# Kernel optimization log

Measured on AMD Instinct MI355X. Metric: run time of the kernel, lower is better.

Reference implementation:

```python
import jax, jax.numpy as jnp
import numpy as np

NPOINT = 2048
K = 16
EPS = 1e-5


def farthest_point_sample(xyz, npoint):
    # xyz: (B, N, 3) -> (B, npoint) int32 indices. Deterministic start at index 0.
    B, N, _ = xyz.shape
    batch = jnp.arange(B)

    def step(carry, _):
        dists, far = carry                      # (B,N), (B,)
        centroid = xyz[batch, far]              # (B,3)
        d = jnp.sum((xyz - centroid[:, None, :]) ** 2, axis=-1)  # (B,N)
        dists = jnp.minimum(dists, d)
        nxt = jnp.argmax(dists, axis=-1).astype(jnp.int32)
        return (dists, nxt), far

    init = (jnp.full((B, N), 1e10, xyz.dtype), jnp.zeros((B,), jnp.int32))
    _, idx = jax.lax.scan(step, init, None, length=npoint)
    return jnp.transpose(idx)                   # (B, npoint)


def knn_query(k, xyz, query_xyz):
    # squared-distance KNN via matmul form (same ordering as torch.cdist+topk smallest)
    x2 = jnp.sum(xyz * xyz, axis=-1)            # (B,N)
    q2 = jnp.sum(query_xyz * query_xyz, axis=-1)  # (B,S)
    sqd = q2[:, :, None] + x2[:, None, :] - 2.0 * jnp.einsum('bsd,bnd->bsn', query_xyz, xyz)
    _, idx = jax.lax.top_k(-sqd, k)             # smallest k distances
    return idx                                  # (B,S,k)


def layer_norm(x, g, b):
    mu = jnp.mean(x, axis=-1, keepdims=True)
    var = jnp.mean((x - mu) ** 2, axis=-1, keepdims=True)
    return (x - mu) * jax.lax.rsqrt(var + EPS) * g + b


def setup_inputs() -> dict:
    key = jax.random.key(0)
    ks = jax.random.split(key, 6)
    B, N, IN_DIM, OUT_DIM = 4, 8192, 64, 128
    C_IN = 3 + IN_DIM
    s1 = 1.0 / np.sqrt(C_IN)
    s2 = 1.0 / np.sqrt(OUT_DIM)
    return {
        'xyz': jax.random.normal(ks[0], (B, N, 3), jnp.float32),
        'feat': jax.random.normal(ks[1], (B, N, IN_DIM), jnp.float32),
        'W1': jax.random.uniform(ks[2], (C_IN, OUT_DIM), jnp.float32, -s1, s1),
        'b1': jax.random.uniform(ks[3], (OUT_DIM,), jnp.float32, -s1, s1),
        'W2': jax.random.uniform(ks[4], (OUT_DIM, OUT_DIM), jnp.float32, -s2, s2),
        'b2': jax.random.uniform(ks[5], (OUT_DIM,), jnp.float32, -s2, s2),
        'ln_g': jnp.ones((OUT_DIM,), jnp.float32),
        'ln_b': jnp.zeros((OUT_DIM,), jnp.float32),
    }


def reference(xyz, feat, W1, b1, W2, b2, ln_g, ln_b):
    B = xyz.shape[0]
    bidx = jnp.arange(B)[:, None, None]

    fps_idx = farthest_point_sample(xyz, NPOINT)                 # (B,S)
    new_xyz = jnp.take_along_axis(xyz, fps_idx[:, :, None], axis=1)  # (B,S,3)
    knn_idx = knn_query(K, xyz, new_xyz)                         # (B,S,K)

    grp_xyz = xyz[bidx, knn_idx] - new_xyz[:, :, None, :]        # (B,S,K,3)
    grp_feat = feat[bidx, knn_idx]                               # (B,S,K,in_dim)
    grouped = jnp.concatenate([grp_xyz, grp_feat], axis=-1)      # (B,S,K,3+in_dim)

    h = jax.nn.relu(grouped @ W1 + b1)
    h = h @ W2 + b2                                              # (B,S,K,out_dim)
    new_feat = jnp.max(h, axis=2)                                # (B,S,out_dim)
    return new_xyz, layer_norm(new_feat, ln_g, ln_b)
```

## Files before the change

kernel.cpp:

```cpp
#include <hip/hip_runtime.h>
#include <stdint.h>

#define BB 4
#define NN 8192
#define SS 2048
#define KK 16
#define IND 64
#define CIN 67
#define OD 128

typedef unsigned int   u32;
typedef unsigned long long u64;
typedef float f2 __attribute__((ext_vector_type(2)));

__global__ __launch_bounds__(256) void k_prep(const float* __restrict__ xyz,
                                              float4* __restrict__ pts){
  int i = blockIdx.x * 256 + threadIdx.x;
  if (i >= BB*NN) return;
  float x = xyz[3*i+0];
  float y = xyz[3*i+1];
  float z = xyz[3*i+2];
  float x2 = __fadd_rn(__fadd_rn(__fmul_rn(x,x), __fmul_rn(y,y)), __fmul_rn(z,z));
  pts[i] = make_float4(x,y,z,x2);
}

template<int CTRL>
__device__ __forceinline__ float dpp_mv(float x){
  int xi = __builtin_bit_cast(int, x);
  int r  = __builtin_amdgcn_update_dpp(xi, xi, CTRL, 0xf, 0xf, false);
  return __builtin_bit_cast(float, r);
}

#define FPT 512
#define PPT (NN/FPT)
#define NW  (FPT/64)
#define FPS_LDS ((3*NN + 3*SS)*4)
__global__ __launch_bounds__(FPT, 2) void k_fps(const float4* __restrict__ pts,
                                                float* __restrict__ out_xyz){
  #pragma clang fp contract(off)
  extern __shared__ float smem[];
  float* sx = smem;
  float* sy = smem +   NN;
  float* sz = smem + 2*NN;
  float* rx = smem + 3*NN;
  float* ry = smem + 3*NN +   SS;
  float* rz = smem + 3*NN + 2*SS;
  __shared__ u64 pkey[2][NW];
  int b = blockIdx.x;
  int tid = threadIdx.x;
  int wid = tid >> 6, lane = tid & 63;
  const float4* P = pts + (size_t)b*NN;
  f2 X[PPT/2], Y[PPT/2], Z[PPT/2], D[PPT/2];
  #pragma unroll
  for (int jp=0;jp<PPT/2;jp++){
    int n0 = tid*PPT + 2*jp;
    float4 p0 = P[n0];
    float4 p1 = P[n0+1];
    X[jp] = (f2){p0.x, p1.x};
    Y[jp] = (f2){p0.y, p1.y};
    Z[jp] = (f2){p0.z, p1.z};
    D[jp] = (f2){1e10f, 1e10f};
    sx[n0]=p0.x; sx[n0+1]=p1.x;
    sy[n0]=p0.y; sy[n0+1]=p1.y;
    sz[n0]=p0.z; sz[n0+1]=p1.z;
  }
  float4 p0v = P[0];
  float cx=p0v.x, cy=p0v.y, cz=p0v.z;
  if (tid==0){ rx[0]=cx; ry[0]=cy; rz[0]=cz; }
  __syncthreads();

  for (int it=1; it<SS; ++it){
    f2 mm = (f2){-1.0f, -1.0f};
    #pragma unroll
    for (int jp=0;jp<PPT/2;jp++){
      f2 dx = X[jp] - cx;
      f2 dy = Y[jp] - cy;
      f2 dz = Z[jp] - cz;
      f2 d  = ((dx*dx) + (dy*dy)) + (dz*dz);
      f2 nd = __builtin_elementwise_min(D[jp], d);
      D[jp] = nd;
      mm = __builtin_elementwise_max(mm, nd);
    }
    float md = fmaxf(mm.x, mm.y);
    float m = md;
    m = fmaxf(m, dpp_mv<0x111>(m));
    m = fmaxf(m, dpp_mv<0x112>(m));
    m = fmaxf(m, dpp_mv<0x114>(m));
    m = fmaxf(m, dpp_mv<0x118>(m));
    m = fmaxf(m, dpp_mv<0x142>(m));
    m = fmaxf(m, dpp_mv<0x143>(m));
    float wmax = __builtin_bit_cast(float,
        __builtin_amdgcn_readlane(__builtin_bit_cast(int, m), 63));
    u64 ball = __ballot(md == wmax);
    int wl = __ffsll((unsigned long long)ball) - 1;
    int bj = 0;
    if (md == wmax){
      #pragma unroll
      for (int t=PPT-1;t>=0;--t){
        float v = (t&1)? D[t>>1].y : D[t>>1].x;
        if (v == wmax) bj = t;
      }
    }
    int widx = __shfl(tid*PPT + bj, wl, 64);
    if (lane==0){
      pkey[it&1][wid] = ((u64)__float_as_uint(wmax) << 32) | (u32)~(u32)widx;
    }
    __syncthreads();
    u64 bk = pkey[it&1][0];
    #pragma unroll
    for (int w=1;w<NW;w++){
      u64 k2 = pkey[it&1][w];
      if (k2 > bk) bk = k2;
    }
    int gw = (int)~(u32)bk;
    cx = sx[gw]; cy = sy[gw]; cz = sz[gw];
    if (tid==0){ rx[it]=cx; ry[it]=cy; rz[it]=cz; }
  }
  __syncthreads();
  for (int i=tid; i<SS; i+=FPT){
    size_t o = (size_t)b*SS*3 + (size_t)i*3;
    out_xyz[o]=rx[i]; out_xyz[o+1]=ry[i]; out_xyz[o+2]=rz[i];
  }
}

__global__ __launch_bounds__(256) void k_knn(const float4* __restrict__ pts,
                                             const float* __restrict__ ctr,
                                             int* __restrict__ knn_idx){
  int q = blockIdx.x*4 + (threadIdx.x>>6);
  int lane = threadIdx.x & 63;
  int b = q / SS;
  const float4* P = pts + (size_t)b*NN;
  float qx=ctr[3*q], qy=ctr[3*q+1], qz=ctr[3*q+2];
  float q2 = __fadd_rn(__fadd_rn(__fmul_rn(qx,qx),__fmul_rn(qy,qy)),__fmul_rn(qz,qz));
  u64 key[KK];
  #pragma unroll
  for (int t=0;t<KK;t++) key[t] = ~0ull;
  for (int i=0;i<NN/64;i++){
    int n = i*64 + lane;
    float4 p = P[n];
    float dot = __fadd_rn(__fadd_rn(__fmul_rn(qx,p.x),__fmul_rn(qy,p.y)),__fmul_rn(qz,p.z));
    float sd  = __fsub_rn(__fadd_rn(q2,p.w), __fmul_rn(2.0f,dot));
    u32 bu = __float_as_uint(sd);
    bu ^= (u32)((int)bu >> 31) | 0x80000000u;
    u64 kk = ((u64)bu<<32) | (u32)n;
    if (kk < key[KK-1]){
      key[KK-1] = kk;
      #pragma unroll
      for (int t=KK-1;t>0;--t){
        u64 a=key[t-1], c=key[t];
        bool sw = c < a;
        key[t-1] = sw? c : a;
        key[t]   = sw? a : c;
      }
    }
  }
  #pragma unroll 1
  for (int r=0;r<KK;r++){
    u64 m = key[0];
    #pragma unroll
    for (int mm=1;mm<64;mm<<=1){
      u64 om = __shfl_xor((unsigned long long)m, mm, 64);
      if (om < m) m = om;
    }
    if (lane==0) knn_idx[q*KK + r] = (int)(u32)m;
    if (key[0]==m){
      #pragma unroll
      for (int t=0;t<KK-1;t++) key[t]=key[t+1];
      key[KK-1]=~0ull;
    }
  }
}

__global__ __launch_bounds__(256) void k_mlp(const float* __restrict__ feat,
                                             const float4* __restrict__ pts,
                                             const float* __restrict__ ctr,
                                             const int* __restrict__ knn_idx,
                                             const float* __restrict__ W1, const float* __restrict__ b1,
                                             const float* __restrict__ W2, const float* __restrict__ b2,
                                             const float* __restrict__ g_ln, const float* __restrict__ b_ln,
                                             float* __restrict__ out_feat){
  __shared__ float gbuf[4][CIN][16];
  __shared__ float hbuf[4][OD][20];
  int wid = threadIdx.x>>6, lane = threadIdx.x&63;
  int q = blockIdx.x*4 + wid;
  int b = q / SS;
  float* gw = &gbuf[wid][0][0];
  float* hw = &hbuf[wid][0][0];
  int k = lane & 15, part = lane >> 4;
  int n = knn_idx[q*KK + k];
  {
    const float* fp = feat + ((size_t)b*NN + (size_t)n)*IND + part*16;
    float4 f0 = *(const float4*)(fp+0);
    float4 f1 = *(const float4*)(fp+4);
    float4 f2v = *(const float4*)(fp+8);
    float4 f3 = *(const float4*)(fp+12);
    float v[16] = {f0.x,f0.y,f0.z,f0.w, f1.x,f1.y,f1.z,f1.w,
                   f2v.x,f2v.y,f2v.z,f2v.w, f3.x,f3.y,f3.z,f3.w};
    #pragma unroll
    for (int c=0;c<16;c++) gw[(3+part*16+c)*16 + k] = v[c];
    if (part==0){
      float4 p = pts[(size_t)b*NN + n];
      gw[0*16+k] = __fsub_rn(p.x, ctr[3*q+0]);
      gw[1*16+k] = __fsub_rn(p.y, ctr[3*q+1]);
      gw[2*16+k] = __fsub_rn(p.z, ctr[3*q+2]);
    }
  }
  __syncthreads();
  int o = lane;
  float a0[16], a1[16];
  #pragma unroll
  for (int t=0;t<16;t++){ a0[t]=0.0f; a1[t]=0.0f; }
  #pragma unroll 4
  for (int j=0;j<CIN;j++){
    float w0 = W1[j*OD + o];
    float w1 = W1[j*OD + o + 64];
    #pragma unroll
    for (int t=0;t<16;t++){
      float gv = gw[j*16+t];
      a0[t]=fmaf(gv,w0,a0[t]); a1[t]=fmaf(gv,w1,a1[t]);
    }
  }
  float bb0 = b1[o], bb1 = b1[o+64];
  #pragma unroll
  for (int t=0;t<16;t++){
    hw[o*20+t]      = fmaxf(a0[t]+bb0, 0.0f);
    hw[(o+64)*20+t] = fmaxf(a1[t]+bb1, 0.0f);
  }
  __syncthreads();
  float c0[16], c1[16];
  #pragma unroll
  for (int t=0;t<16;t++){ c0[t]=0.0f; c1[t]=0.0f; }
  #pragma unroll 4
  for (int j=0;j<OD;j++){
    float w0 = W2[j*OD + o];
    float w1 = W2[j*OD + o + 64];
    #pragma unroll
    for (int t=0;t<16;t++){
      float hv = hw[j*20+t];
      c0[t]=fmaf(hv,w0,c0[t]); c1[t]=fmaf(hv,w1,c1[t]);
    }
  }
  float m0=c0[0], m1=c1[0];
  #pragma unroll
  for (int t=1;t<16;t++){ m0=fmaxf(m0,c0[t]); m1=fmaxf(m1,c1[t]); }
  m0 += b2[o]; m1 += b2[o+64];
  float ssum = m0+m1;
  #pragma unroll
  for (int mm=1;mm<64;mm<<=1) ssum += __shfl_xor(ssum,mm,64);
  float mean = ssum * (1.0f/128.0f);
  float d0=m0-mean, d1=m1-mean;
  float sq = d0*d0 + d1*d1;
  #pragma unroll
  for (int mm=1;mm<64;mm<<=1) sq += __shfl_xor(sq,mm,64);
  float var = sq * (1.0f/128.0f);
  float x = var + 1e-5f;
  float r = rsqrtf(x);
  r = r * (1.5f - 0.5f*x*r*r);
  size_t obf = (size_t)q*OD;
  out_feat[obf+o]    = fmaf(d0*r, g_ln[o],    b_ln[o]);
  out_feat[obf+o+64] = fmaf(d1*r, g_ln[o+64], b_ln[o+64]);
}

extern "C" void kernel_launch(void* const* d_in, const int* in_sizes, int n_in,
                              void* d_out, int out_size, void* d_ws, size_t ws_size,
                              hipStream_t stream){
  const float* xyz  = (const float*)d_in[0];
  const float* feat = (const float*)d_in[1];
  const float* W1   = (const float*)d_in[2];
  const float* b1   = (const float*)d_in[3];
  const float* W2   = (const float*)d_in[4];
  const float* b2   = (const float*)d_in[5];
  const float* lg   = (const float*)d_in[6];
  const float* lb   = (const float*)d_in[7];
  float* out = (float*)d_out;
  char* ws = (char*)d_ws;
  float4* pts = (float4*)ws;
  int*    kidx = (int*)(ws + 524288);
  float* out_xyz  = out;
  float* out_feat = out + (size_t)BB*SS*3;

  hipFuncSetAttribute((const void*)k_fps,
                      hipFuncAttributeMaxDynamicSharedMemorySize, FPS_LDS);

  hipLaunchKernelGGL(k_prep, dim3((BB*NN+255)/256), dim3(256), 0,       stream, xyz, pts);
  hipLaunchKernelGGL(k_fps,  dim3(BB),              dim3(FPT), FPS_LDS, stream, pts, out_xyz);
  hipLaunchKernelGGL(k_knn,  dim3(BB*SS/4),         dim3(256), 0,       stream, pts, out_xyz, kidx);
  hipLaunchKernelGGL(k_mlp,  dim3(BB*SS/4),         dim3(256), 0,       stream,
                     feat, pts, out_xyz, kidx, W1, b1, W2, b2, lg, lb, out_feat);
}
```

Before: 2.408 ms.

## Halve FPS block size, split max accumulators, and drop shuffle in argmax

The farthest-point-sampling kernel now runs with 256 threads per batch instead of 512, so each thread holds 32 points and there are 4 waves instead of 8. The per-iteration cross-wave reduction and barrier therefore involve fewer participants. The distance loop uses two independent max accumulators to shorten the dependency chain. The winning lane writes its key directly instead of going through a shuffle, and the 4-wave key reduction is written as a tree. In exchange, each thread does twice the per-iteration distance work and needs more registers, which could lengthen the serial critical path of the 2048-iteration loop.

```diff
diff --git a/kernel.cpp b/kernel.cpp
--- a/kernel.cpp
+++ b/kernel.cpp
@@ -31,11 +31,11 @@
   return __builtin_bit_cast(float, r);
 }
 
-#define FPT 512
+#define FPT 256
 #define PPT (NN/FPT)
 #define NW  (FPT/64)
 #define FPS_LDS ((3*NN + 3*SS)*4)
-__global__ __launch_bounds__(FPT, 2) void k_fps(const float4* __restrict__ pts,
+__global__ __launch_bounds__(FPT, 1) void k_fps(const float4* __restrict__ pts,
                                                 float* __restrict__ out_xyz){
   #pragma clang fp contract(off)
   extern __shared__ float smem[];
@@ -70,17 +70,21 @@
   __syncthreads();
 
   for (int it=1; it<SS; ++it){
-    f2 mm = (f2){-1.0f, -1.0f};
-    #pragma unroll
-    for (int jp=0;jp<PPT/2;jp++){
-      f2 dx = X[jp] - cx;
-      f2 dy = Y[jp] - cy;
-      f2 dz = Z[jp] - cz;
-      f2 d  = ((dx*dx) + (dy*dy)) + (dz*dz);
-      f2 nd = __builtin_elementwise_min(D[jp], d);
-      D[jp] = nd;
-      mm = __builtin_elementwise_max(mm, nd);
-    }
+    f2 mm0 = (f2){-1.0f, -1.0f}, mm1 = (f2){-1.0f, -1.0f};
+    #pragma unroll
+    for (int jp=0;jp<PPT/2;jp+=2){
+      f2 dx0 = X[jp] - cx,   dy0 = Y[jp] - cy,   dz0 = Z[jp] - cz;
+      f2 dx1 = X[jp+1] - cx, dy1 = Y[jp+1] - cy, dz1 = Z[jp+1] - cz;
+      f2 d0  = ((dx0*dx0) + (dy0*dy0)) + (dz0*dz0);
+      f2 d1  = ((dx1*dx1) + (dy1*dy1)) + (dz1*dz1);
+      f2 nd0 = __builtin_elementwise_min(D[jp],   d0);
+      f2 nd1 = __builtin_elementwise_min(D[jp+1], d1);
+      D[jp]   = nd0;
+      D[jp+1] = nd1;
+      mm0 = __builtin_elementwise_max(mm0, nd0);
+      mm1 = __builtin_elementwise_max(mm1, nd1);
+    }
+    f2 mm = __builtin_elementwise_max(mm0, mm1);
     float md = fmaxf(mm.x, mm.y);
     float m = md;
     m = fmaxf(m, dpp_mv<0x111>(m));
@@ -93,25 +97,22 @@
         __builtin_amdgcn_readlane(__builtin_bit_cast(int, m), 63));
     u64 ball = __ballot(md == wmax);
     int wl = __ffsll((unsigned long long)ball) - 1;
-    int bj = 0;
-    if (md == wmax){
+    if (lane == wl){
+      int bj = 0;
       #pragma unroll
       for (int t=PPT-1;t>=0;--t){
         float v = (t&1)? D[t>>1].y : D[t>>1].x;
         if (v == wmax) bj = t;
       }
-    }
-    int widx = __shfl(tid*PPT + bj, wl, 64);
-    if (lane==0){
+      int widx = tid*PPT + bj;
       pkey[it&1][wid] = ((u64)__float_as_uint(wmax) << 32) | (u32)~(u32)widx;
     }
     __syncthreads();
-    u64 bk = pkey[it&1][0];
-    #pragma unroll
-    for (int w=1;w<NW;w++){
-      u64 k2 = pkey[it&1][w];
-      if (k2 > bk) bk = k2;
-    }
+    u64 k0 = pkey[it&1][0], k1 = pkey[it&1][1];
+    u64 k2 = pkey[it&1][2], k3 = pkey[it&1][3];
+    u64 ka = k0 > k1 ? k0 : k1;
+    u64 kb = k2 > k3 ? k2 : k3;
+    u64 bk = ka > kb ? ka : kb;
     int gw = (int)~(u32)bk;
     cx = sx[gw]; cy = sy[gw]; cz = sz[gw];
     if (tid==0){ rx[it]=cx; ry[it]=cy; rz[it]=cz; }
```

After: 2.849 ms. +18.3%, slower.
